# Performance work log

Measured on AMD Instinct MI355X. Metric: run time of the kernel, lower is better.

## Reference

```python
import jax, jax.numpy as jnp
import numpy as np

PERIODS = (7, 30, 90)
KEEP_ORIGINAL = True
DROP_NA = False
T, F = 262144, 64


def setup_inputs() -> dict:
    key = jax.random.key(0)
    x = jax.random.normal(key, (T, F), dtype=jnp.float32)
    return {"x": x}


def _moving_average(x, cumsum, period):
    # drop_na=False path of _compute_ma:
    #   i <  period-1 : cumsum[i] / (i+1)   (i==0 gives x[0], same as cumsum[0]/1)
    #   i >= period-1 : (cumsum[i] - cumsum[i-period]) / period, with cumsum[i-period]=0 at i==period-1
    t = x.shape[0]
    idx = jnp.arange(t)
    shifted = jnp.concatenate(
        [jnp.zeros((period,) + x.shape[1:], dtype=x.dtype), cumsum[:-period]], axis=0
    )
    windowed = (cumsum - shifted) / jnp.asarray(period, x.dtype)
    expanding = cumsum / (idx + 1).astype(x.dtype)[:, None]
    return jnp.where((idx >= period - 1)[:, None], windowed, expanding)


def reference(x):
    cumsum = jnp.cumsum(x, axis=0)  # shared prefix sum across all periods
    parts = [x] if KEEP_ORIGINAL else []
    for p in PERIODS:
        parts.append(_moving_average(x, cumsum, p))
    # drop_na=False -> all parts have length T, min_batch_size = T
    return jnp.concatenate(parts, axis=-1)  # [T, (1+len(PERIODS))*F]
```

## Files before the change

### kernel.cpp

```cpp
#include <hip/hip_runtime.h>


#define T_ROWS 262144
#define F_COLS 64
#define OUT_COLS 256
#define CHUNK 128
#define CHUNKS_PER_BLOCK 4

__global__ __launch_bounds__(256) void ma_kernel(const float* __restrict__ x,
                                                 float* __restrict__ out) {
    const int tid   = threadIdx.x;
    const int col   = tid & 63;
    const int chunk = blockIdx.x * CHUNKS_PER_BLOCK + (tid >> 6);
    const long r0   = (long)chunk * CHUNK;

    const float* __restrict__ xc = x + col;
    float* __restrict__ oc = out + col;

    float s7 = 0.f, s30 = 0.f, s90 = 0.f;

    if (chunk == 0) {
        for (int i = 0; i < CHUNK; ++i) {
            float v = xc[(long)i * F_COLS];
            s7 += v; s30 += v; s90 += v;
            if (i >= 7)  s7  -= xc[(long)(i - 7)  * F_COLS];
            if (i >= 30) s30 -= xc[(long)(i - 30) * F_COLS];
            if (i >= 90) s90 -= xc[(long)(i - 90) * F_COLS];
            float d7  = (i < 6)  ? (float)(i + 1) : 7.f;
            float d30 = (i < 29) ? (float)(i + 1) : 30.f;
            float d90 = (i < 89) ? (float)(i + 1) : 90.f;
            long ob = (long)i * OUT_COLS;
            oc[ob]       = v;
            oc[ob + 64]  = s7  / d7;
            oc[ob + 128] = s30 / d30;
            oc[ob + 192] = s90 / d90;
        }
    } else {
        #pragma unroll
        for (int k = 1; k <= 7; ++k) {
            float v = xc[(r0 - k) * F_COLS];
            s7 += v; s30 += v; s90 += v;
        }
        #pragma unroll
        for (int k = 8; k <= 30; ++k) {
            float v = xc[(r0 - k) * F_COLS];
            s30 += v; s90 += v;
        }
        #pragma unroll 2
        for (int k = 31; k <= 90; ++k) {
            s90 += xc[(r0 - k) * F_COLS];
        }

        const float r7 = 1.f / 7.f, r30 = 1.f / 30.f, r90 = 1.f / 90.f;
        #pragma unroll 4
        for (int i = 0; i < CHUNK; ++i) {
            const long gi = r0 + i;
            float v   = xc[gi * F_COLS];
            float o7  = xc[(gi - 7)  * F_COLS];
            float o30 = xc[(gi - 30) * F_COLS];
            float o90 = xc[(gi - 90) * F_COLS];
            s7  += v - o7;
            s30 += v - o30;
            s90 += v - o90;
            const long ob = gi * OUT_COLS;
            oc[ob]       = v;
            oc[ob + 64]  = s7  * r7;
            oc[ob + 128] = s30 * r30;
            oc[ob + 192] = s90 * r90;
        }
    }
}

extern "C" void kernel_launch(void* const* d_in, const int* in_sizes, int n_in,
                              void* d_out, int out_size, void* d_ws, size_t ws_size,
                              hipStream_t stream) {
    const float* x = (const float*)d_in[0];
    float* out = (float*)d_out;
    const int n_chunks = T_ROWS / CHUNK;
    const int n_blocks = n_chunks / CHUNKS_PER_BLOCK;
    ma_kernel<<<n_blocks, 256, 0, stream>>>(x, out);
}
```

Baseline: 368.8 us.

## Vectorize moving-average kernel with float4 and shrink chunks to 32 rows

Each thread now handles four adjacent columns through float4 loads and stores, so 16 lanes cover a row and each wave processes four chunks. The chunk size drops from 128 to 32 rows, which raises parallelism (8192 chunks) but makes the 90-row warmup prefix proportionally larger, increasing redundant reads of x. The first chunks, whose start row is below 90, take a reduced-precision division path that replays from row zero. The aim is wider memory transactions and more blocks to saturate bandwidth, in exchange for extra reads.

```diff
diff --git a/kernel.cpp b/kernel.cpp
--- a/kernel.cpp
+++ b/kernel.cpp
@@ -2,71 +2,87 @@
 
 
 #define T_ROWS 262144
-#define F_COLS 64
-#define OUT_COLS 256
-#define CHUNK 128
-#define CHUNKS_PER_BLOCK 4
+#define CHUNK 32
+#define XSTRIDE4 16
+#define OSTRIDE4 64
 
-__global__ __launch_bounds__(256) void ma_kernel(const float* __restrict__ x,
-                                                 float* __restrict__ out) {
-    const int tid   = threadIdx.x;
-    const int col   = tid & 63;
-    const int chunk = blockIdx.x * CHUNKS_PER_BLOCK + (tid >> 6);
-    const long r0   = (long)chunk * CHUNK;
+__device__ __forceinline__ float4 f4add(float4 a, float4 b) {
+    return make_float4(a.x + b.x, a.y + b.y, a.z + b.z, a.w + b.w);
+}
+__device__ __forceinline__ float4 f4sub(float4 a, float4 b) {
+    return make_float4(a.x - b.x, a.y - b.y, a.z - b.z, a.w - b.w);
+}
+__device__ __forceinline__ float4 f4scale(float4 a, float s) {
+    return make_float4(a.x * s, a.y * s, a.z * s, a.w * s);
+}
 
-    const float* __restrict__ xc = x + col;
-    float* __restrict__ oc = out + col;
+__global__ __launch_bounds__(256) void ma_kernel(const float4* __restrict__ x,
+                                                 float4* __restrict__ out) {
+    const int tid  = threadIdx.x;
+    const int lane = tid & 63;
+    const int wave = tid >> 6;
+    const int sub  = lane >> 4;
+    const int c    = lane & 15;
 
-    float s7 = 0.f, s30 = 0.f, s90 = 0.f;
+    const int chunk = (blockIdx.x * 4 + wave) * 4 + sub;
+    const int r0 = chunk * CHUNK;
 
-    if (chunk == 0) {
-        for (int i = 0; i < CHUNK; ++i) {
-            float v = xc[(long)i * F_COLS];
-            s7 += v; s30 += v; s90 += v;
-            if (i >= 7)  s7  -= xc[(long)(i - 7)  * F_COLS];
-            if (i >= 30) s30 -= xc[(long)(i - 30) * F_COLS];
-            if (i >= 90) s90 -= xc[(long)(i - 90) * F_COLS];
-            float d7  = (i < 6)  ? (float)(i + 1) : 7.f;
-            float d30 = (i < 29) ? (float)(i + 1) : 30.f;
-            float d90 = (i < 89) ? (float)(i + 1) : 90.f;
-            long ob = (long)i * OUT_COLS;
-            oc[ob]       = v;
-            oc[ob + 64]  = s7  / d7;
-            oc[ob + 128] = s30 / d30;
-            oc[ob + 192] = s90 / d90;
-        }
-    } else {
+    const float4* __restrict__ xc = x + c;
+    float4* __restrict__ oc = out + c;
+
+    float4 s7  = make_float4(0.f, 0.f, 0.f, 0.f);
+    float4 s30 = s7, s90 = s7;
+
+    if (r0 >= 90) {
         #pragma unroll
         for (int k = 1; k <= 7; ++k) {
-            float v = xc[(r0 - k) * F_COLS];
-            s7 += v; s30 += v; s90 += v;
+            float4 v = xc[(r0 - k) * XSTRIDE4];
+            s7 = f4add(s7, v); s30 = f4add(s30, v); s90 = f4add(s90, v);
         }
         #pragma unroll
         for (int k = 8; k <= 30; ++k) {
-            float v = xc[(r0 - k) * F_COLS];
-            s30 += v; s90 += v;
+            float4 v = xc[(r0 - k) * XSTRIDE4];
+            s30 = f4add(s30, v); s90 = f4add(s90, v);
         }
-        #pragma unroll 2
+        #pragma unroll 6
         for (int k = 31; k <= 90; ++k) {
-            s90 += xc[(r0 - k) * F_COLS];
+            s90 = f4add(s90, xc[(r0 - k) * XSTRIDE4]);
         }
 
-        const float r7 = 1.f / 7.f, r30 = 1.f / 30.f, r90 = 1.f / 90.f;
+        const float r7i = 1.f / 7.f, r30i = 1.f / 30.f, r90i = 1.f / 90.f;
         #pragma unroll 4
         for (int i = 0; i < CHUNK; ++i) {
-            const long gi = r0 + i;
-            float v   = xc[gi * F_COLS];
-            float o7  = xc[(gi - 7)  * F_COLS];
-            float o30 = xc[(gi - 30) * F_COLS];
-            float o90 = xc[(gi - 90) * F_COLS];
-            s7  += v - o7;
-            s30 += v - o30;
-            s90 += v - o90;
-            const long ob = gi * OUT_COLS;
-            oc[ob]       = v;
-            oc[ob + 64]  = s7  * r7;
-            oc[ob + 128] = s30 * r30;
-            oc[ob + 192] = s90 * r90;
+            const int gi = r0 + i;
+            float4 v   = xc[gi * XSTRIDE4];
+            float4 o7  = xc[(gi - 7)  * XSTRIDE4];
+            float4 o30 = xc[(gi - 30) * XSTRIDE4];
+            float4 o90 = xc[(gi - 90) * XSTRIDE4];
+            s7  = f4add(s7,  f4sub(v, o7));
+            s30 = f4add(s30, f4sub(v, o30));
+            s90 = f4add(s90, f4sub(v, o90));
+            const int ob = gi * OSTRIDE4;
+            oc[ob]      = v;
+            oc[ob + 16] = f4scale(s7,  r7i);
+            oc[ob + 32] = f4scale(s30, r30i);
+            oc[ob + 48] = f4scale(s90, r90i);
+        }
+    } else {
+        for (int i = 0; i < r0 + CHUNK; ++i) {
+            float4 v = xc[i * XSTRIDE4];
+            s7 = f4add(s7, v); s30 = f4add(s30, v); s90 = f4add(s90, v);
+            if (i >= 7)  s7  = f4sub(s7,  xc[(i - 7)  * XSTRIDE4]);
+            if (i >= 30) s30 = f4sub(s30, xc[(i - 30) * XSTRIDE4]);
+            if (i >= 90) s90 = f4sub(s90, xc[(i - 90) * XSTRIDE4]);
+            if (i >= r0) {
+                float d7  = (i < 6)  ? 1.f / (float)(i + 1) : 1.f / 7.f;
+                float d30 = (i < 29) ? 1.f / (float)(i + 1) : 1.f / 30.f;
+                float d90 = (i < 89) ? 1.f / (float)(i + 1) : 1.f / 90.f;
+                const int ob = i * OSTRIDE4;
+                oc[ob]      = v;
+                oc[ob + 16] = f4scale(s7,  d7);
+                oc[ob + 32] = f4scale(s30, d30);
+                oc[ob + 48] = f4scale(s90, d90);
+            }
         }
     }
 }
@@ -74,9 +90,9 @@
 extern "C" void kernel_launch(void* const* d_in, const int* in_sizes, int n_in,
                               void* d_out, int out_size, void* d_ws, size_t ws_size,
                               hipStream_t stream) {
-    const float* x = (const float*)d_in[0];
-    float* out = (float*)d_out;
+    const float4* x = (const float4*)d_in[0];
+    float4* out = (float4*)d_out;
     const int n_chunks = T_ROWS / CHUNK;
-    const int n_blocks = n_chunks / CHUNKS_PER_BLOCK;
+    const int n_blocks = n_chunks / 16;
     ma_kernel<<<n_blocks, 256, 0, stream>>>(x, out);
 }
```

Result: no change. 374.2 us (+1.5%).
